# Kernel tuning notes

Hardware: AMD Instinct MI355X
Metric: run time of the kernel (lower is better)

Reference implementation:

```python
import jax, jax.numpy as jnp
import numpy as np

N, D_IN, D_HID, D_OUT, E = 8192, 1024, 4096, 1024, 8

def setup_inputs() -> dict:
    key = jax.random.key(0)
    ks = jax.random.split(key, 5)
    s_in = 1.0 / np.sqrt(D_IN)
    s_hid = 1.0 / np.sqrt(D_HID)
    return {
        "x": jax.random.normal(ks[0], (N, D_IN), dtype=jnp.float32),
        "W1": jax.random.normal(ks[1], (E, D_IN, D_HID), dtype=jnp.float32) * s_in,
        "b1": jnp.zeros((E, D_HID), dtype=jnp.float32),
        "W2": jax.random.normal(ks[2], (E, D_HID, D_OUT), dtype=jnp.float32) * s_hid,
        "b2": jnp.zeros((E, D_OUT), dtype=jnp.float32),
        "Wg": jax.random.normal(ks[3], (D_IN, E), dtype=jnp.float32) * s_in,
        "bg": jnp.zeros((E,), dtype=jnp.float32),
        "k": 2,
    }

def reference(x, W1, b1, W2, b2, Wg, bg, k):
    # Gating: softmax over ALL experts, then mask to top-k and renormalize
    scores = x @ Wg + bg                      # [N, E]
    _, topk_idx = jax.lax.top_k(scores, k)    # [N, k]
    mask = jax.nn.one_hot(topk_idx, scores.shape[-1], dtype=scores.dtype).sum(-2)  # [N, E]
    w = jax.nn.softmax(scores, axis=-1) * mask
    w = w / (w.sum(-1, keepdims=True) + 1e-8)  # [N, E]
    # Dense compute-all-experts (faithful to torch.stack over experts)
    h = jax.nn.relu(jnp.einsum('ni,eih->enh', x, W1) + b1[:, None, :])  # [E, N, hid]
    outs = jnp.einsum('enh,eho->eno', h, W2) + b2[:, None, :]           # [E, N, out]
    # Weighted combine over experts
    return jnp.einsum('ne,eno->no', w, outs)   # [N, out]
```

## Files before the change

### kernel.cpp

```cpp
#include <hip/hip_runtime.h>
#include <hip/hip_bf16.h>
#include <stdint.h>

#define N_TOK 8192
#define DIN   1024
#define DHID  4096
#define DOUT  1024
#define NE    8

typedef __attribute__((ext_vector_type(8))) __bf16 bf16x8;
typedef __attribute__((ext_vector_type(4))) float  f32x4;
typedef __attribute__((ext_vector_type(8))) unsigned short u16x8;

__device__ __forceinline__ unsigned short f2bfu(float f) {
    union { float f; unsigned u; } a; a.f = f;
    unsigned r = a.u + 0x7FFF + ((a.u >> 16) & 1);
    return (unsigned short)(r >> 16);
}

__device__ __forceinline__ void gload_lds16(const void* g, void* l) {
    __builtin_amdgcn_global_load_lds(
        (__attribute__((address_space(1))) void*)(void*)g,
        (__attribute__((address_space(3))) void*)l,
        16, 0, 0);
}

__global__ void transpose_cast_kernel(const float* __restrict__ in, unsigned short* __restrict__ out,
                                      int R, int C) {
    __shared__ float t[64][65];
    const size_t RC = (size_t)R * C;
    const float* ine = in + (size_t)blockIdx.z * RC;
    unsigned short* oute = out + (size_t)blockIdx.z * RC;
    int c0 = blockIdx.x * 64, r0 = blockIdx.y * 64;
    int tid = threadIdx.x;
    #pragma unroll
    for (int it = 0; it < 4; it++) {
        int idx = it * 256 + tid;
        int r = idx >> 4, cq = (idx & 15) * 4;
        float4 v = *(const float4*)(ine + (size_t)(r0 + r) * C + c0 + cq);
        t[r][cq] = v.x; t[r][cq + 1] = v.y; t[r][cq + 2] = v.z; t[r][cq + 3] = v.w;
    }
    __syncthreads();
    #pragma unroll
    for (int it = 0; it < 2; it++) {
        int u = it * 256 + tid;
        int c = u >> 3, g = (u & 7) * 8;
        u16x8 o;
        #pragma unroll
        for (int v = 0; v < 8; v++) o[v] = f2bfu(t[g + v][c]);
        *(u16x8*)(oute + (size_t)(c0 + c) * R + r0 + g) = o;
    }
}

__global__ void gate_kernel(const float* __restrict__ x, const float* __restrict__ Wg,
                            const float* __restrict__ bg, int* __restrict__ counts,
                            int* __restrict__ tok_list, int* __restrict__ slot_list,
                            float* __restrict__ wslot, unsigned short* __restrict__ xb) {
    int wv = threadIdx.x >> 6, lane = threadIdx.x & 63;
    int n = blockIdx.x * 4 + wv;
    float acc[NE];
    #pragma unroll
    for (int e = 0; e < NE; e++) acc[e] = 0.f;
    const float* xr = x + (size_t)n * DIN;
    unsigned short* xbr = xb + (size_t)n * DIN;
    #pragma unroll
    for (int i = 0; i < DIN / 256; i++) {
        int d = i * 256 + lane * 4;
        float4 xv = *(const float4*)(xr + d);
        ushort4 o;
        o.x = f2bfu(xv.x); o.y = f2bfu(xv.y); o.z = f2bfu(xv.z); o.w = f2bfu(xv.w);
        *(ushort4*)(xbr + d) = o;
        const float* w = Wg + (size_t)d * NE;
        #pragma unroll
        for (int u = 0; u < 4; u++) {
            float xs = (&xv.x)[u];
            float4 w0 = *(const float4*)(w + u * NE);
            float4 w1 = *(const float4*)(w + u * NE + 4);
            acc[0] += xs * w0.x; acc[1] += xs * w0.y; acc[2] += xs * w0.z; acc[3] += xs * w0.w;
            acc[4] += xs * w1.x; acc[5] += xs * w1.y; acc[6] += xs * w1.z; acc[7] += xs * w1.w;
        }
    }
    #pragma unroll
    for (int off = 32; off; off >>= 1)
        #pragma unroll
        for (int e = 0; e < NE; e++) acc[e] += __shfl_down(acc[e], off);
    if (lane == 0) {
        float s[NE], p[NE];
        float mx = -1e30f;
        #pragma unroll
        for (int e = 0; e < NE; e++) { s[e] = acc[e] + bg[e]; mx = fmaxf(mx, s[e]); }
        float sum = 0.f;
        #pragma unroll
        for (int e = 0; e < NE; e++) { p[e] = expf(s[e] - mx); sum += p[e]; }
        float inv = 1.f / sum;
        int e0 = 0;
        #pragma unroll
        for (int e = 1; e < NE; e++) if (s[e] > s[e0]) e0 = e;
        int e1 = (e0 == 0) ? 1 : 0;
        #pragma unroll
        for (int e = 0; e < NE; e++) if (e != e0 && s[e] > s[e1]) e1 = e;
        float p0 = p[e0] * inv, p1 = p[e1] * inv;
        float rn = 1.f / (p0 + p1 + 1e-8f);
        int pos0 = atomicAdd(&counts[e0], 1);
        tok_list[e0 * N_TOK + pos0] = n; slot_list[e0 * N_TOK + pos0] = 2 * n;     wslot[e0 * N_TOK + pos0] = p0 * rn;
        int pos1 = atomicAdd(&counts[e1], 1);
        tok_list[e1 * N_TOK + pos1] = n; slot_list[e1 * N_TOK + pos1] = 2 * n + 1; wslot[e1 * N_TOK + pos1] = p1 * rn;
    }
}

template <int KDIM, int NDIM, bool IS_GEMM1>
__global__ __launch_bounds__(256, 4)
void moe_gemm(const unsigned short* __restrict__ Asrc, const unsigned short* __restrict__ Bt,
              const float* __restrict__ bias, unsigned short* __restrict__ Hdst,
              float* __restrict__ Odst, const int* __restrict__ counts,
              const int* __restrict__ tok_list, const int* __restrict__ slot_list,
              const float* __restrict__ wslot) {
    constexpr int NT_N = NDIM / 128;
    int ell = blockIdx.x;
    int e = ell & 7;
    int s = ell >> 3;
    int tile_n = s % NT_N;
    int tile_m = s / NT_N;
    int count = counts[e];
    if (tile_m * 128 >= count) return;

    __shared__ __align__(16) unsigned short As[128 * 64];
    __shared__ __align__(16) unsigned short Bs[128 * 64];
    __shared__ int rowid_s[128];
    __shared__ int outid_s[128];
    __shared__ float w_s[128];

    int tid = threadIdx.x;
    if (tid < 128) {
        int r = tile_m * 128 + tid;
        int rr = (r < count) ? r : tile_m * 128;
        int base = e * N_TOK + rr;
        if (IS_GEMM1) { rowid_s[tid] = tok_list[base]; outid_s[tid] = slot_list[base]; }
        else          { rowid_s[tid] = slot_list[base]; outid_s[tid] = tok_list[base]; w_s[tid] = wslot[base]; }
    }
    __syncthreads();

    int lane = tid & 63;
    int wv = tid >> 6;

    int ric = lane >> 3;
    int k8  = (lane & 7) ^ ric;
    const unsigned short* aptr[4];
    const unsigned short* bptr[4];
    #pragma unroll
    for (int i = 0; i < 4; i++) {
        int c = wv * 4 + i;
        int row = c * 8 + ric;
        aptr[i] = Asrc + (size_t)rowid_s[row] * KDIM + k8 * 8;
        bptr[i] = Bt + ((size_t)e * NDIM + tile_n * 128 + row) * KDIM + k8 * 8;
    }

    f32x4 acc[4][4];
    #pragma unroll
    for (int i = 0; i < 4; i++)
        #pragma unroll
        for (int j = 0; j < 4; j++) acc[i][j] = (f32x4){0.f, 0.f, 0.f, 0.f};

    int wm = (wv >> 1) * 64, wn = (wv & 1) * 64;
    int r16 = lane & 15, quad = lane >> 4;

    for (int kk = 0; kk < KDIM / 64; kk++) {
        #pragma unroll
        for (int i = 0; i < 4; i++) {
            gload_lds16(aptr[i] + kk * 64, (void*)(As + (wv * 4 + i) * 512));
            gload_lds16(bptr[i] + kk * 64, (void*)(Bs + (wv * 4 + i) * 512));
        }
        __syncthreads();
        #pragma unroll
        for (int kh = 0; kh < 2; kh++) {
            int swk = ((kh * 4 + quad) ^ (r16 & 7)) * 8;
            bf16x8 av[4], bv[4];
            #pragma unroll
            for (int i = 0; i < 4; i++)
                av[i] = *(const bf16x8*)(As + (wm + i * 16 + r16) * 64 + swk);
            #pragma unroll
            for (int j = 0; j < 4; j++)
                bv[j] = *(const bf16x8*)(Bs + (wn + j * 16 + r16) * 64 + swk);
            #pragma unroll
            for (int i = 0; i < 4; i++)
                #pragma unroll
                for (int j = 0; j < 4; j++)
                    acc[i][j] = __builtin_amdgcn_mfma_f32_16x16x32_bf16(av[i], bv[j], acc[i][j], 0, 0, 0);
        }
        __syncthreads();
    }

    float bias_r[4];
    #pragma unroll
    for (int j = 0; j < 4; j++)
        bias_r[j] = bias[(size_t)e * NDIM + tile_n * 128 + wn + j * 16 + r16];
    #pragma unroll
    for (int i = 0; i < 4; i++) {
        #pragma unroll
        for (int reg = 0; reg < 4; reg++) {
            int r = wm + i * 16 + quad * 4 + reg;
            if (tile_m * 128 + r >= count) continue;
            #pragma unroll
            for (int j = 0; j < 4; j++) {
                int col = tile_n * 128 + wn + j * 16 + r16;
                float v = acc[i][j][reg] + bias_r[j];
                if (IS_GEMM1) {
                    v = fmaxf(v, 0.f);
                    Hdst[(size_t)outid_s[r] * NDIM + col] = f2bfu(v);
                } else {
                    atomicAdd(&Odst[(size_t)outid_s[r] * NDIM + col], w_s[r] * v);
                }
            }
        }
    }
}

extern "C" void kernel_launch(void* const* d_in, const int* in_sizes, int n_in,
                              void* d_out, int out_size, void* d_ws, size_t ws_size,
                              hipStream_t stream) {
    const float* x  = (const float*)d_in[0];
    const float* W1 = (const float*)d_in[1];
    const float* b1 = (const float*)d_in[2];
    const float* W2 = (const float*)d_in[3];
    const float* b2 = (const float*)d_in[4];
    const float* Wg = (const float*)d_in[5];
    const float* bg = (const float*)d_in[6];
    float* out = (float*)d_out;

    char* ws = (char*)d_ws;
    unsigned short* xb  = (unsigned short*)(ws + 0);
    unsigned short* w1t = (unsigned short*)(ws + 16777216);
    unsigned short* w2t = (unsigned short*)(ws + 83886080);
    unsigned short* h   = (unsigned short*)(ws + 150994944);
    int*   counts    = (int*)(ws + 285212672);
    int*   tok_list  = (int*)(ws + 285212928);
    int*   slot_list = (int*)(ws + 285475072);
    float* wslot     = (float*)(ws + 285737216);

    hipMemsetAsync(counts, 0, 256, stream);
    hipMemsetAsync(d_out, 0, (size_t)out_size * sizeof(float), stream);

    transpose_cast_kernel<<<dim3(DHID / 64, DIN / 64, NE), 256, 0, stream>>>(W1, w1t, DIN, DHID);
    transpose_cast_kernel<<<dim3(DOUT / 64, DHID / 64, NE), 256, 0, stream>>>(W2, w2t, DHID, DOUT);
    gate_kernel<<<N_TOK / 4, 256, 0, stream>>>(x, Wg, bg, counts, tok_list, slot_list, wslot, xb);

    moe_gemm<DIN, DHID, true><<<NE * (N_TOK / 128) * (DHID / 128), 256, 0, stream>>>(
        xb, w1t, b1, h, nullptr, counts, tok_list, slot_list, wslot);
    moe_gemm<DHID, DOUT, false><<<NE * (N_TOK / 128) * (DOUT / 128), 256, 0, stream>>>(
        h, w2t, b2, nullptr, out, counts, tok_list, slot_list, wslot);
}
```

Baseline: 896.2 us.

## Use persistent per-expert grid with split-K for second MoE GEMM

```diff
diff --git a/kernel.cpp b/kernel.cpp
--- a/kernel.cpp
+++ b/kernel.cpp
@@ -108,7 +108,7 @@
     }
 }
 
-template <int KDIM, int NDIM, bool IS_GEMM1>
+template <int KDIM, int NDIM, bool IS_GEMM1, int SPLITK>
 __global__ __launch_bounds__(256, 4)
 void moe_gemm(const unsigned short* __restrict__ Asrc, const unsigned short* __restrict__ Bt,
               const float* __restrict__ bias, unsigned short* __restrict__ Hdst,
@@ -116,13 +116,12 @@
               const int* __restrict__ tok_list, const int* __restrict__ slot_list,
               const float* __restrict__ wslot) {
     constexpr int NT_N = NDIM / 128;
-    int ell = blockIdx.x;
-    int e = ell & 7;
-    int s = ell >> 3;
-    int tile_n = s % NT_N;
-    int tile_m = s / NT_N;
+    constexpr int NT_M = N_TOK / 128;
+    constexpr int KLEN = KDIM / SPLITK;
+
+    int e = blockIdx.x & 7;
+    int local = blockIdx.x >> 3;
     int count = counts[e];
-    if (tile_m * 128 >= count) return;
 
     __shared__ __align__(16) unsigned short As[128 * 64];
     __shared__ __align__(16) unsigned short Bs[128 * 64];
@@ -131,84 +130,95 @@
     __shared__ float w_s[128];
 
     int tid = threadIdx.x;
-    if (tid < 128) {
-        int r = tile_m * 128 + tid;
-        int rr = (r < count) ? r : tile_m * 128;
-        int base = e * N_TOK + rr;
-        if (IS_GEMM1) { rowid_s[tid] = tok_list[base]; outid_s[tid] = slot_list[base]; }
-        else          { rowid_s[tid] = slot_list[base]; outid_s[tid] = tok_list[base]; w_s[tid] = wslot[base]; }
-    }
-    __syncthreads();
-
     int lane = tid & 63;
     int wv = tid >> 6;
-
     int ric = lane >> 3;
     int k8  = (lane & 7) ^ ric;
-    const unsigned short* aptr[4];
-    const unsigned short* bptr[4];
-    #pragma unroll
-    for (int i = 0; i < 4; i++) {
-        int c = wv * 4 + i;
-        int row = c * 8 + ric;
-        aptr[i] = Asrc + (size_t)rowid_s[row] * KDIM + k8 * 8;
-        bptr[i] = Bt + ((size_t)e * NDIM + tile_n * 128 + row) * KDIM + k8 * 8;
-    }
-
-    f32x4 acc[4][4];
-    #pragma unroll
-    for (int i = 0; i < 4; i++)
-        #pragma unroll
-        for (int j = 0; j < 4; j++) acc[i][j] = (f32x4){0.f, 0.f, 0.f, 0.f};
-
     int wm = (wv >> 1) * 64, wn = (wv & 1) * 64;
     int r16 = lane & 15, quad = lane >> 4;
 
-    for (int kk = 0; kk < KDIM / 64; kk++) {
+    for (int w = local; ; w += 128) {
+        int tile_n = w % NT_N;
+        int r = w / NT_N;
+        int kh = r % SPLITK;
+        int tile_m = r / SPLITK;
+        if (tile_m >= NT_M) break;
+        if (tile_m * 128 >= count) break;
+
+        __syncthreads();
+        if (tid < 128) {
+            int rr = tile_m * 128 + tid;
+            if (rr >= count) rr = tile_m * 128;
+            int base = e * N_TOK + rr;
+            if (IS_GEMM1) { rowid_s[tid] = tok_list[base]; outid_s[tid] = slot_list[base]; }
+            else          { rowid_s[tid] = slot_list[base]; outid_s[tid] = tok_list[base]; w_s[tid] = wslot[base]; }
+        }
+        __syncthreads();
+
+        const int k0 = kh * KLEN;
+        const unsigned short* aptr[4];
+        const unsigned short* bptr[4];
         #pragma unroll
         for (int i = 0; i < 4; i++) {
-            gload_lds16(aptr[i] + kk * 64, (void*)(As + (wv * 4 + i) * 512));
-            gload_lds16(bptr[i] + kk * 64, (void*)(Bs + (wv * 4 + i) * 512));
-        }
-        __syncthreads();
-        #pragma unroll
-        for (int kh = 0; kh < 2; kh++) {
-            int swk = ((kh * 4 + quad) ^ (r16 & 7)) * 8;
-            bf16x8 av[4], bv[4];
-            #pragma unroll
-            for (int i = 0; i < 4; i++)
-                av[i] = *(const bf16x8*)(As + (wm + i * 16 + r16) * 64 + swk);
-            #pragma unroll
-            for (int j = 0; j < 4; j++)
-                bv[j] = *(const bf16x8*)(Bs + (wn + j * 16 + r16) * 64 + swk);
-            #pragma unroll
-            for (int i = 0; i < 4; i++)
+            int c = wv * 4 + i;
+            int row = c * 8 + ric;
+            aptr[i] = Asrc + (size_t)rowid_s[row] * KDIM + k0 + k8 * 8;
+            bptr[i] = Bt + ((size_t)e * NDIM + tile_n * 128 + row) * KDIM + k0 + k8 * 8;
+        }
+
+        f32x4 acc[4][4];
+        #pragma unroll
+        for (int i = 0; i < 4; i++)
+            #pragma unroll
+            for (int j = 0; j < 4; j++) acc[i][j] = (f32x4){0.f, 0.f, 0.f, 0.f};
+
+        for (int kk = 0; kk < KLEN / 64; kk++) {
+            #pragma unroll
+            for (int i = 0; i < 4; i++) {
+                gload_lds16(aptr[i] + kk * 64, (void*)(As + (wv * 4 + i) * 512));
+                gload_lds16(bptr[i] + kk * 64, (void*)(Bs + (wv * 4 + i) * 512));
+            }
+            __syncthreads();
+            #pragma unroll
+            for (int kh2 = 0; kh2 < 2; kh2++) {
+                int swk = ((kh2 * 4 + quad) ^ (r16 & 7)) * 8;
+                bf16x8 av[4], bv[4];
+                #pragma unroll
+                for (int i = 0; i < 4; i++)
+                    av[i] = *(const bf16x8*)(As + (wm + i * 16 + r16) * 64 + swk);
                 #pragma unroll
                 for (int j = 0; j < 4; j++)
-                    acc[i][j] = __builtin_amdgcn_mfma_f32_16x16x32_bf16(av[i], bv[j], acc[i][j], 0, 0, 0);
-        }
-        __syncthreads();
-    }
-
-    float bias_r[4];
-    #pragma unroll
-    for (int j = 0; j < 4; j++)
-        bias_r[j] = bias[(size_t)e * NDIM + tile_n * 128 + wn + j * 16 + r16];
-    #pragma unroll
-    for (int i = 0; i < 4; i++) {
-        #pragma unroll
-        for (int reg = 0; reg < 4; reg++) {
-            int r = wm + i * 16 + quad * 4 + reg;
-            if (tile_m * 128 + r >= count) continue;
-            #pragma unroll
-            for (int j = 0; j < 4; j++) {
-                int col = tile_n * 128 + wn + j * 16 + r16;
-                float v = acc[i][j][reg] + bias_r[j];
-                if (IS_GEMM1) {
-                    v = fmaxf(v, 0.f);
-                    Hdst[(size_t)outid_s[r] * NDIM + col] = f2bfu(v);
-                } else {
-                    atomicAdd(&Odst[(size_t)outid_s[r] * NDIM + col], w_s[r] * v);
+                    bv[j] = *(const bf16x8*)(Bs + (wn + j * 16 + r16) * 64 + swk);
+                #pragma unroll
+                for (int i = 0; i < 4; i++)
+                    #pragma unroll
+                    for (int j = 0; j < 4; j++)
+                        acc[i][j] = __builtin_amdgcn_mfma_f32_16x16x32_bf16(av[i], bv[j], acc[i][j], 0, 0, 0);
+            }
+            __syncthreads();
+        }
+
+        float bias_r[4];
+        #pragma unroll
+        for (int j = 0; j < 4; j++)
+            bias_r[j] = bias[(size_t)e * NDIM + tile_n * 128 + wn + j * 16 + r16];
+        #pragma unroll
+        for (int i = 0; i < 4; i++) {
+            #pragma unroll
+            for (int reg = 0; reg < 4; reg++) {
+                int rr = wm + i * 16 + quad * 4 + reg;
+                if (tile_m * 128 + rr >= count) continue;
+                #pragma unroll
+                for (int j = 0; j < 4; j++) {
+                    int col = tile_n * 128 + wn + j * 16 + r16;
+                    float v = acc[i][j][reg];
+                    if (IS_GEMM1) {
+                        v = fmaxf(v + bias_r[j], 0.f);
+                        Hdst[(size_t)outid_s[rr] * NDIM + col] = f2bfu(v);
+                    } else {
+                        if (kh == 0) v += bias_r[j];
+                        atomicAdd(&Odst[(size_t)outid_s[rr] * NDIM + col], w_s[rr] * v);
+                    }
                 }
             }
         }
@@ -244,8 +254,8 @@
     transpose_cast_kernel<<<dim3(DOUT / 64, DHID / 64, NE), 256, 0, stream>>>(W2, w2t, DHID, DOUT);
     gate_kernel<<<N_TOK / 4, 256, 0, stream>>>(x, Wg, bg, counts, tok_list, slot_list, wslot, xb);
 
-    moe_gemm<DIN, DHID, true><<<NE * (N_TOK / 128) * (DHID / 128), 256, 0, stream>>>(
+    moe_gemm<DIN, DHID, true, 1><<<1024, 256, 0, stream>>>(
         xb, w1t, b1, h, nullptr, counts, tok_list, slot_list, wslot);
-    moe_gemm<DHID, DOUT, false><<<NE * (N_TOK / 128) * (DOUT / 128), 256, 0, stream>>>(
+    moe_gemm<DHID, DOUT, false, 2><<<1024, 256, 0, stream>>>(
         h, w2t, b2, nullptr, out, counts, tok_list, slot_list, wslot);
 }
```

Measured after the change: 889.6 us. Within noise of the previous version (-0.7%).
